# Performance work log

Hardware: AMD Instinct MI355X
Metric: run time of the kernel (lower is better)

Reference implementation:

```python
import jax, jax.numpy as jnp
import numpy as np

N_NODES = 100000
N_EDGES = 3200000
IN_CH = 128
HID = 32


def setup_inputs() -> dict:
    key = jax.random.key(0)
    ks = jax.random.split(key, 8)
    x = jax.random.normal(ks[0], (N_NODES, IN_CH), dtype=jnp.float32)
    edge_index = jax.random.randint(ks[1], (2, N_EDGES), 0, N_NODES, dtype=jnp.int64)
    # Glorot-ish scaled weights
    W1 = jax.random.normal(ks[2], (IN_CH, HID), dtype=jnp.float32) / np.sqrt(IN_CH)
    b1 = jnp.zeros((HID,), dtype=jnp.float32)
    W2 = jax.random.normal(ks[3], (HID, HID), dtype=jnp.float32) / np.sqrt(HID)
    b2 = jnp.zeros((HID,), dtype=jnp.float32)
    Wc = jax.random.normal(ks[4], (HID, 2), dtype=jnp.float32) / np.sqrt(HID)
    bc = jnp.zeros((2,), dtype=jnp.float32)
    return {"x": x, "edge_index": edge_index, "W1": W1, "b1": b1,
            "W2": W2, "b2": b2, "Wc": Wc, "bc": bc}


def _gcn_norm(edge_index, n_nodes):
    # PyG GCNConv default: add self-loops, symmetric normalization
    src, dst = edge_index[0], edge_index[1]
    loops = jnp.arange(n_nodes, dtype=src.dtype)
    src = jnp.concatenate([src, loops])
    dst = jnp.concatenate([dst, loops])
    deg = jax.ops.segment_sum(jnp.ones_like(dst, dtype=jnp.float32), dst,
                              num_segments=n_nodes)
    dis = jnp.where(deg > 0, jax.lax.rsqrt(deg), 0.0)  # deg^{-1/2}
    norm = dis[src] * dis[dst]                          # [E + N]
    return src, dst, norm


def _gcn_conv(x, W, b, src, dst, norm, n_nodes):
    h = x @ W                                   # [N, out] linear first (out <= in)
    msg = h[src] * norm[:, None]                # gather + scale  [E+N, out]
    out = jax.ops.segment_sum(msg, dst, num_segments=n_nodes)  # scatter-add
    return out + b


def reference(x, edge_index, W1, b1, W2, b2, Wc, bc):
    n = x.shape[0]
    src, dst, norm = _gcn_norm(edge_index, n)
    h = jax.nn.relu(_gcn_conv(x, W1, b1, src, dst, norm, n))
    h = jax.nn.relu(_gcn_conv(h, W2, b2, src, dst, norm, n))
    return h @ Wc + bc                          # [N, 2]
```

## Files before the change

kernel.cpp:

```cpp
#include <hip/hip_runtime.h>

#define NCH 32
#define INCH 128
#define SH 7
#define BNODES 128
#define CAP 4544
#define P1_CHUNK 8192
#define NBINS_PAD 1024
#define HCH 16

__device__ __forceinline__ unsigned int pack_bf16x2(float a, float b) {
  unsigned int ua = __float_as_uint(a);
  unsigned int ub = __float_as_uint(b);
  ua = (ua + 0x7FFFu + ((ua >> 16) & 1u)) >> 16;
  ub = (ub + 0x7FFFu + ((ub >> 16) & 1u)) & 0xFFFF0000u;
  return ub | ua;
}
__device__ __forceinline__ float lo_bf16(unsigned int u) { return __uint_as_float(u << 16); }
__device__ __forceinline__ float hi_bf16(unsigned int u) { return __uint_as_float(u & 0xFFFF0000u); }

__global__ void k_initcur(int* gcur, int nbk) {
  int i = blockIdx.x * blockDim.x + threadIdx.x;
  if (i < nbk) gcur[i] = i * CAP;
}

__global__ __launch_bounds__(256) void k_part(const int* __restrict__ ei, int* gcur,
                                              unsigned int* __restrict__ srcsb, int E) {
  __shared__ unsigned int sorted[P1_CHUNK];
  __shared__ int hist[NBINS_PAD];
  __shared__ int bbase[NBINS_PAD + 1];
  __shared__ int bfill[NBINS_PAD];
  __shared__ int wsums[4];
  const int tid = threadIdx.x;
  const int base = blockIdx.x * P1_CHUNK;
  const int cnt = min(P1_CHUNK, E - base);

  for (int i = tid; i < NBINS_PAD; i += 256) hist[i] = 0;
  __syncthreads();
  for (int i = tid; i < cnt; i += 256) {
    int d = ei[E + base + i];
    atomicAdd(&hist[d >> SH], 1);
  }
  __syncthreads();
  int c0 = hist[4 * tid], c1 = hist[4 * tid + 1], c2 = hist[4 * tid + 2], c3 = hist[4 * tid + 3];
  int s = c0 + c1 + c2 + c3;
  int lane = tid & 63, w = tid >> 6;
  int incl = s;
#pragma unroll
  for (int off = 1; off < 64; off <<= 1) {
    int t = __shfl_up(incl, off, 64);
    if (lane >= off) incl += t;
  }
  if (lane == 63) wsums[w] = incl;
  __syncthreads();
  int woff = 0;
  for (int i = 0; i < w; ++i) woff += wsums[i];
  int te = woff + incl - s;
  bbase[4 * tid] = te;                     bfill[4 * tid] = te;
  bbase[4 * tid + 1] = te + c0;            bfill[4 * tid + 1] = te + c0;
  bbase[4 * tid + 2] = te + c0 + c1;       bfill[4 * tid + 2] = te + c0 + c1;
  bbase[4 * tid + 3] = te + c0 + c1 + c2;  bfill[4 * tid + 3] = te + c0 + c1 + c2;
  if (tid == 255) bbase[NBINS_PAD] = te + s;
  __syncthreads();
  for (int i = tid; i < cnt; i += 256) {
    int d = ei[E + base + i];
    int srcv = ei[base + i];
    int b = d >> SH;
    int pos = atomicAdd(&bfill[b], 1);
    sorted[pos] = ((unsigned int)(d & (BNODES - 1)) << 17) | (unsigned int)srcv;
  }
  __syncthreads();
  for (int b = tid; b < NBINS_PAD; b += 256) {
    int c = bbase[b + 1] - bbase[b];
    hist[b] = (c > 0) ? atomicAdd(&gcur[b], c) : 0;
  }
  __syncthreads();
  for (int i = tid; i < cnt; i += 256) {
    int lo = 0, hi = NBINS_PAD - 1;
#pragma unroll
    for (int it = 0; it < 10; ++it) {
      int mid = (lo + hi + 1) >> 1;
      if (bbase[mid] <= i) lo = mid; else hi = mid - 1;
    }
    int gpos = hist[lo] + (i - bbase[lo]);
    if (gpos < (lo + 1) * CAP) srcsb[gpos] = sorted[i];
  }
}

__global__ __launch_bounds__(256) void k_bsort(const int* __restrict__ gcur,
                                               unsigned int* __restrict__ srcsb,
                                               int* __restrict__ rowbeg, int* __restrict__ rowend,
                                               float* __restrict__ dis, int N) {
  __shared__ unsigned int raw[CAP];
  __shared__ unsigned int sbuf[CAP];
  __shared__ int hist2[BNODES];
  __shared__ int sc[BNODES];
  __shared__ int fill2[BNODES];
  const int tid = threadIdx.x;
  const int bin = blockIdx.x;
  const int base = bin * CAP;
  int cnt = min(gcur[bin] - base, CAP);

  if (tid < BNODES) hist2[tid] = 0;
  for (int i = tid; i < cnt; i += 256) raw[i] = srcsb[base + i];
  __syncthreads();
  for (int i = tid; i < cnt; i += 256) atomicAdd(&hist2[raw[i] >> 17], 1);
  __syncthreads();
  int deg = (tid < BNODES) ? hist2[tid] : 0;
  if (tid < BNODES) sc[tid] = deg;
  __syncthreads();
  for (int off = 1; off < BNODES; off <<= 1) {
    int t = 0;
    if (tid < BNODES && tid >= off) t = sc[tid - off];
    __syncthreads();
    if (tid < BNODES) sc[tid] += t;
    __syncthreads();
  }
  int excl = 0;
  if (tid < BNODES) { excl = sc[tid] - deg; fill2[tid] = excl; }
  __syncthreads();
  for (int i = tid; i < cnt; i += 256) {
    unsigned int v = raw[i];
    int pos = atomicAdd(&fill2[v >> 17], 1);
    sbuf[pos] = v & 0x1FFFFu;
  }
  __syncthreads();
  for (int i = tid; i < cnt; i += 256) srcsb[base + i] = sbuf[i];
  if (tid < BNODES) {
    int n = bin * BNODES + tid;
    if (n < N) {
      rowbeg[n] = base + excl;
      rowend[n] = base + excl + deg;
      dis[n] = rsqrtf((float)(deg + 1));
    }
  }
}

__global__ __launch_bounds__(256) void k_gemm1(const float* __restrict__ x,
                                               const float* __restrict__ W1,
                                               const float* __restrict__ dis,
                                               unsigned int* __restrict__ hs, int N) {
  __shared__ float w[INCH * NCH];
  for (int i = threadIdx.x; i < INCH * NCH; i += blockDim.x) w[i] = W1[i];
  __syncthreads();
  int n = blockIdx.x * 16 + (threadIdx.x >> 4);
  int c2 = threadIdx.x & 15;
  if (n >= N) return;
  const float* xr = x + (size_t)n * INCH;
  float ax = 0.f, ay = 0.f;
#pragma unroll
  for (int k = 0; k < INCH; ++k) {
    float xv = xr[k];
    float2 ww = ((const float2*)(w + k * NCH))[c2];
    ax = fmaf(xv, ww.x, ax);
    ay = fmaf(xv, ww.y, ay);
  }
  float dn = dis[n];
  hs[(size_t)n * HCH + c2] = pack_bf16x2(ax * dn, ay * dn);
}

__global__ __launch_bounds__(256) void k_agg1g2(
    const int* __restrict__ rowbeg, const int* __restrict__ rowend,
    const unsigned int* __restrict__ srcs, const unsigned int* __restrict__ hs,
    const float* __restrict__ dis, const float* __restrict__ b1,
    const float* __restrict__ W2, unsigned int* __restrict__ hs2, int N) {
  __shared__ float w[NCH * NCH];
  for (int i = threadIdx.x; i < NCH * NCH; i += blockDim.x) w[i] = W2[i];
  __syncthreads();
  int n = blockIdx.x * 16 + (threadIdx.x >> 4);
  int c2 = threadIdx.x & 15;
  if (n >= N) return;
  int j = rowbeg[n], end = rowend[n];
  unsigned int su = hs[(size_t)n * HCH + c2];
  float ax = lo_bf16(su), ay = hi_bf16(su);
  for (; j + 8 <= end; j += 8) {
    unsigned int u0 = hs[(size_t)srcs[j] * HCH + c2];
    unsigned int u1 = hs[(size_t)srcs[j + 1] * HCH + c2];
    unsigned int u2 = hs[(size_t)srcs[j + 2] * HCH + c2];
    unsigned int u3 = hs[(size_t)srcs[j + 3] * HCH + c2];
    unsigned int u4 = hs[(size_t)srcs[j + 4] * HCH + c2];
    unsigned int u5 = hs[(size_t)srcs[j + 5] * HCH + c2];
    unsigned int u6 = hs[(size_t)srcs[j + 6] * HCH + c2];
    unsigned int u7 = hs[(size_t)srcs[j + 7] * HCH + c2];
    ax += ((lo_bf16(u0) + lo_bf16(u1)) + (lo_bf16(u2) + lo_bf16(u3))) +
          ((lo_bf16(u4) + lo_bf16(u5)) + (lo_bf16(u6) + lo_bf16(u7)));
    ay += ((hi_bf16(u0) + hi_bf16(u1)) + (hi_bf16(u2) + hi_bf16(u3))) +
          ((hi_bf16(u4) + hi_bf16(u5)) + (hi_bf16(u6) + hi_bf16(u7)));
  }
  for (; j < end; ++j) {
    unsigned int u = hs[(size_t)srcs[j] * HCH + c2];
    ax += lo_bf16(u);
    ay += hi_bf16(u);
  }
  float dn = dis[n];
  float v0 = fmaxf(fmaf(ax, dn, b1[2 * c2]), 0.f);
  float v1 = fmaxf(fmaf(ay, dn, b1[2 * c2 + 1]), 0.f);
  float o0 = 0.f, o1 = 0.f;
#pragma unroll
  for (int k2 = 0; k2 < 16; ++k2) {
    float a = __shfl(v0, k2, 16);
    float b = __shfl(v1, k2, 16);
    float2 wa = ((const float2*)(w + (2 * k2) * NCH))[c2];
    float2 wb = ((const float2*)(w + (2 * k2 + 1) * NCH))[c2];
    o0 = fmaf(a, wa.x, fmaf(b, wb.x, o0));
    o1 = fmaf(a, wa.y, fmaf(b, wb.y, o1));
  }
  hs2[(size_t)n * HCH + c2] = pack_bf16x2(o0 * dn, o1 * dn);
}

__global__ __launch_bounds__(256) void k_agg2h(
    const int* __restrict__ rowbeg, const int* __restrict__ rowend,
    const unsigned int* __restrict__ srcs, const unsigned int* __restrict__ hs2,
    const float* __restrict__ dis, const float* __restrict__ b2,
    const float* __restrict__ Wc, const float* __restrict__ bc,
    float* __restrict__ out, int N) {
  int n = blockIdx.x * 16 + (threadIdx.x >> 4);
  int c2 = threadIdx.x & 15;
  if (n >= N) return;
  int j = rowbeg[n], end = rowend[n];
  unsigned int su = hs2[(size_t)n * HCH + c2];
  float ax = lo_bf16(su), ay = hi_bf16(su);
  for (; j + 8 <= end; j += 8) {
    unsigned int u0 = hs2[(size_t)srcs[j] * HCH + c2];
    unsigned int u1 = hs2[(size_t)srcs[j + 1] * HCH + c2];
    unsigned int u2 = hs2[(size_t)srcs[j + 2] * HCH + c2];
    unsigned int u3 = hs2[(size_t)srcs[j + 3] * HCH + c2];
    unsigned int u4 = hs2[(size_t)srcs[j + 4] * HCH + c2];
    unsigned int u5 = hs2[(size_t)srcs[j + 5] * HCH + c2];
    unsigned int u6 = hs2[(size_t)srcs[j + 6] * HCH + c2];
    unsigned int u7 = hs2[(size_t)srcs[j + 7] * HCH + c2];
    ax += ((lo_bf16(u0) + lo_bf16(u1)) + (lo_bf16(u2) + lo_bf16(u3))) +
          ((lo_bf16(u4) + lo_bf16(u5)) + (lo_bf16(u6) + lo_bf16(u7)));
    ay += ((hi_bf16(u0) + hi_bf16(u1)) + (hi_bf16(u2) + hi_bf16(u3))) +
          ((hi_bf16(u4) + hi_bf16(u5)) + (hi_bf16(u6) + hi_bf16(u7)));
  }
  for (; j < end; ++j) {
    unsigned int u = hs2[(size_t)srcs[j] * HCH + c2];
    ax += lo_bf16(u);
    ay += hi_bf16(u);
  }
  float dn = dis[n];
  float v0 = fmaxf(fmaf(ax, dn, b2[2 * c2]), 0.f);
  float v1 = fmaxf(fmaf(ay, dn, b2[2 * c2 + 1]), 0.f);
  float s0 = v0 * Wc[(2 * c2) * 2 + 0] + v1 * Wc[(2 * c2 + 1) * 2 + 0];
  float s1 = v0 * Wc[(2 * c2) * 2 + 1] + v1 * Wc[(2 * c2 + 1) * 2 + 1];
#pragma unroll
  for (int off = 8; off > 0; off >>= 1) {
    s0 += __shfl_down(s0, off, 16);
    s1 += __shfl_down(s1, off, 16);
  }
  if (c2 == 0) {
    out[(size_t)n * 2 + 0] = s0 + bc[0];
    out[(size_t)n * 2 + 1] = s1 + bc[1];
  }
}

extern "C" void kernel_launch(void* const* d_in, const int* in_sizes, int n_in,
                              void* d_out, int out_size, void* d_ws, size_t ws_size,
                              hipStream_t stream) {
  const float* x  = (const float*)d_in[0];
  const int*   ei = (const int*)d_in[1];
  const float* W1 = (const float*)d_in[2];
  const float* b1 = (const float*)d_in[3];
  const float* W2 = (const float*)d_in[4];
  const float* b2 = (const float*)d_in[5];
  const float* Wc = (const float*)d_in[6];
  const float* bc = (const float*)d_in[7];
  float* out = (float*)d_out;

  const int N = in_sizes[0] / INCH;
  const int E = in_sizes[1] / 2;
  const int nbk = (N + BNODES - 1) / BNODES;

  float*        dis    = (float*)d_ws;
  int*          rowbeg = (int*)(dis + N);
  int*          rowend = rowbeg + N;
  int*          gcur   = rowend + N;
  unsigned int* srcsb  = (unsigned int*)(gcur + nbk);
  unsigned int* bufA   = srcsb + (size_t)nbk * CAP;
  unsigned int* bufB   = bufA + (size_t)N * HCH;

  const int bn = 256;
  const int gP1  = (E + P1_CHUNK - 1) / P1_CHUNK;
  const int gN16 = (N + 15) / 16;

  k_initcur<<<(nbk + bn - 1) / bn, bn, 0, stream>>>(gcur, nbk);
  k_part<<<gP1, bn, 0, stream>>>(ei, gcur, srcsb, E);
  k_bsort<<<nbk, bn, 0, stream>>>(gcur, srcsb, rowbeg, rowend, dis, N);

  k_gemm1<<<gN16, bn, 0, stream>>>(x, W1, dis, bufA, N);
  k_agg1g2<<<gN16, bn, 0, stream>>>(rowbeg, rowend, srcsb, bufA, dis, b1, W2, bufB, N);
  k_agg2h<<<gN16, bn, 0, stream>>>(rowbeg, rowend, srcsb, bufB, dis, b2, Wc, bc, out, N);
}
```

Measured before the change: 212.6 us.

## Split feature tables into channel halves to shrink gather working set

```diff
diff --git a/kernel.cpp b/kernel.cpp
--- a/kernel.cpp
+++ b/kernel.cpp
@@ -7,7 +7,7 @@
 #define CAP 4544
 #define P1_CHUNK 8192
 #define NBINS_PAD 1024
-#define HCH 16
+#define HB 8
 
 __device__ __forceinline__ unsigned int pack_bf16x2(float a, float b) {
   unsigned int ua = __float_as_uint(a);
@@ -139,7 +139,8 @@
 __global__ __launch_bounds__(256) void k_gemm1(const float* __restrict__ x,
                                                const float* __restrict__ W1,
                                                const float* __restrict__ dis,
-                                               unsigned int* __restrict__ hs, int N) {
+                                               unsigned int* __restrict__ hsA,
+                                               unsigned int* __restrict__ hsB, int N) {
   __shared__ float w[INCH * NCH];
   for (int i = threadIdx.x; i < INCH * NCH; i += blockDim.x) w[i] = W1[i];
   __syncthreads();
@@ -156,92 +157,85 @@
     ay = fmaf(xv, ww.y, ay);
   }
   float dn = dis[n];
-  hs[(size_t)n * HCH + c2] = pack_bf16x2(ax * dn, ay * dn);
-}
-
-__global__ __launch_bounds__(256) void k_agg1g2(
+  unsigned int p = pack_bf16x2(ax * dn, ay * dn);
+  if (c2 < 8) hsA[(size_t)n * HB + c2] = p;
+  else        hsB[(size_t)n * HB + (c2 - 8)] = p;
+}
+
+__global__ __launch_bounds__(256) void k_aggh(
     const int* __restrict__ rowbeg, const int* __restrict__ rowend,
-    const unsigned int* __restrict__ srcs, const unsigned int* __restrict__ hs,
-    const float* __restrict__ dis, const float* __restrict__ b1,
-    const float* __restrict__ W2, unsigned int* __restrict__ hs2, int N) {
-  __shared__ float w[NCH * NCH];
-  for (int i = threadIdx.x; i < NCH * NCH; i += blockDim.x) w[i] = W2[i];
-  __syncthreads();
-  int n = blockIdx.x * 16 + (threadIdx.x >> 4);
-  int c2 = threadIdx.x & 15;
+    const unsigned int* __restrict__ srcs, const unsigned int* __restrict__ tbl,
+    float2* __restrict__ acc, int N) {
+  int n = blockIdx.x * 32 + (threadIdx.x >> 3);
+  int c = threadIdx.x & 7;
   if (n >= N) return;
   int j = rowbeg[n], end = rowend[n];
-  unsigned int su = hs[(size_t)n * HCH + c2];
+  unsigned int su = tbl[(size_t)n * HB + c];
   float ax = lo_bf16(su), ay = hi_bf16(su);
   for (; j + 8 <= end; j += 8) {
-    unsigned int u0 = hs[(size_t)srcs[j] * HCH + c2];
-    unsigned int u1 = hs[(size_t)srcs[j + 1] * HCH + c2];
-    unsigned int u2 = hs[(size_t)srcs[j + 2] * HCH + c2];
-    unsigned int u3 = hs[(size_t)srcs[j + 3] * HCH + c2];
-    unsigned int u4 = hs[(size_t)srcs[j + 4] * HCH + c2];
-    unsigned int u5 = hs[(size_t)srcs[j + 5] * HCH + c2];
-    unsigned int u6 = hs[(size_t)srcs[j + 6] * HCH + c2];
-    unsigned int u7 = hs[(size_t)srcs[j + 7] * HCH + c2];
+    unsigned int u0 = tbl[(size_t)srcs[j] * HB + c];
+    unsigned int u1 = tbl[(size_t)srcs[j + 1] * HB + c];
+    unsigned int u2 = tbl[(size_t)srcs[j + 2] * HB + c];
+    unsigned int u3 = tbl[(size_t)srcs[j + 3] * HB + c];
+    unsigned int u4 = tbl[(size_t)srcs[j + 4] * HB + c];
+    unsigned int u5 = tbl[(size_t)srcs[j + 5] * HB + c];
+    unsigned int u6 = tbl[(size_t)srcs[j + 6] * HB + c];
+    unsigned int u7 = tbl[(size_t)srcs[j + 7] * HB + c];
     ax += ((lo_bf16(u0) + lo_bf16(u1)) + (lo_bf16(u2) + lo_bf16(u3))) +
           ((lo_bf16(u4) + lo_bf16(u5)) + (lo_bf16(u6) + lo_bf16(u7)));
     ay += ((hi_bf16(u0) + hi_bf16(u1)) + (hi_bf16(u2) + hi_bf16(u3))) +
           ((hi_bf16(u4) + hi_bf16(u5)) + (hi_bf16(u6) + hi_bf16(u7)));
   }
   for (; j < end; ++j) {
-    unsigned int u = hs[(size_t)srcs[j] * HCH + c2];
+    unsigned int u = tbl[(size_t)srcs[j] * HB + c];
     ax += lo_bf16(u);
     ay += hi_bf16(u);
   }
+  acc[(size_t)n * HB + c] = make_float2(ax, ay);
+}
+
+__global__ __launch_bounds__(256) void k_mlp2(
+    const float2* __restrict__ accA, const float2* __restrict__ accB,
+    const float* __restrict__ dis, const float* __restrict__ b1,
+    const float* __restrict__ W2, unsigned int* __restrict__ hs2A,
+    unsigned int* __restrict__ hs2B, int N) {
+  __shared__ float w[NCH * NCH];
+  for (int i = threadIdx.x; i < NCH * NCH; i += blockDim.x) w[i] = W2[i];
+  __syncthreads();
+  int n = blockIdx.x * 16 + (threadIdx.x >> 4);
+  int c2 = threadIdx.x & 15;
+  if (n >= N) return;
+  float2 a = (c2 < 8) ? accA[(size_t)n * HB + c2] : accB[(size_t)n * HB + (c2 - 8)];
   float dn = dis[n];
-  float v0 = fmaxf(fmaf(ax, dn, b1[2 * c2]), 0.f);
-  float v1 = fmaxf(fmaf(ay, dn, b1[2 * c2 + 1]), 0.f);
+  float v0 = fmaxf(fmaf(a.x, dn, b1[2 * c2]), 0.f);
+  float v1 = fmaxf(fmaf(a.y, dn, b1[2 * c2 + 1]), 0.f);
   float o0 = 0.f, o1 = 0.f;
 #pragma unroll
   for (int k2 = 0; k2 < 16; ++k2) {
-    float a = __shfl(v0, k2, 16);
-    float b = __shfl(v1, k2, 16);
+    float va = __shfl(v0, k2, 16);
+    float vb = __shfl(v1, k2, 16);
     float2 wa = ((const float2*)(w + (2 * k2) * NCH))[c2];
     float2 wb = ((const float2*)(w + (2 * k2 + 1) * NCH))[c2];
-    o0 = fmaf(a, wa.x, fmaf(b, wb.x, o0));
-    o1 = fmaf(a, wa.y, fmaf(b, wb.y, o1));
-  }
-  hs2[(size_t)n * HCH + c2] = pack_bf16x2(o0 * dn, o1 * dn);
-}
-
-__global__ __launch_bounds__(256) void k_agg2h(
-    const int* __restrict__ rowbeg, const int* __restrict__ rowend,
-    const unsigned int* __restrict__ srcs, const unsigned int* __restrict__ hs2,
+    o0 = fmaf(va, wa.x, fmaf(vb, wb.x, o0));
+    o1 = fmaf(va, wa.y, fmaf(vb, wb.y, o1));
+  }
+  unsigned int p = pack_bf16x2(o0 * dn, o1 * dn);
+  if (c2 < 8) hs2A[(size_t)n * HB + c2] = p;
+  else        hs2B[(size_t)n * HB + (c2 - 8)] = p;
+}
+
+__global__ __launch_bounds__(256) void k_head(
+    const float2* __restrict__ accA, const float2* __restrict__ accB,
     const float* __restrict__ dis, const float* __restrict__ b2,
     const float* __restrict__ Wc, const float* __restrict__ bc,
     float* __restrict__ out, int N) {
   int n = blockIdx.x * 16 + (threadIdx.x >> 4);
   int c2 = threadIdx.x & 15;
   if (n >= N) return;
-  int j = rowbeg[n], end = rowend[n];
-  unsigned int su = hs2[(size_t)n * HCH + c2];
-  float ax = lo_bf16(su), ay = hi_bf16(su);
-  for (; j + 8 <= end; j += 8) {
-    unsigned int u0 = hs2[(size_t)srcs[j] * HCH + c2];
-    unsigned int u1 = hs2[(size_t)srcs[j + 1] * HCH + c2];
-    unsigned int u2 = hs2[(size_t)srcs[j + 2] * HCH + c2];
-    unsigned int u3 = hs2[(size_t)srcs[j + 3] * HCH + c2];
-    unsigned int u4 = hs2[(size_t)srcs[j + 4] * HCH + c2];
-    unsigned int u5 = hs2[(size_t)srcs[j + 5] * HCH + c2];
-    unsigned int u6 = hs2[(size_t)srcs[j + 6] * HCH + c2];
-    unsigned int u7 = hs2[(size_t)srcs[j + 7] * HCH + c2];
-    ax += ((lo_bf16(u0) + lo_bf16(u1)) + (lo_bf16(u2) + lo_bf16(u3))) +
-          ((lo_bf16(u4) + lo_bf16(u5)) + (lo_bf16(u6) + lo_bf16(u7)));
-    ay += ((hi_bf16(u0) + hi_bf16(u1)) + (hi_bf16(u2) + hi_bf16(u3))) +
-          ((hi_bf16(u4) + hi_bf16(u5)) + (hi_bf16(u6) + hi_bf16(u7)));
-  }
-  for (; j < end; ++j) {
-    unsigned int u = hs2[(size_t)srcs[j] * HCH + c2];
-    ax += lo_bf16(u);
-    ay += hi_bf16(u);
-  }
+  float2 a = (c2 < 8) ? accA[(size_t)n * HB + c2] : accB[(size_t)n * HB + (c2 - 8)];
   float dn = dis[n];
-  float v0 = fmaxf(fmaf(ax, dn, b2[2 * c2]), 0.f);
-  float v1 = fmaxf(fmaf(ay, dn, b2[2 * c2 + 1]), 0.f);
+  float v0 = fmaxf(fmaf(a.x, dn, b2[2 * c2]), 0.f);
+  float v1 = fmaxf(fmaf(a.y, dn, b2[2 * c2 + 1]), 0.f);
   float s0 = v0 * Wc[(2 * c2) * 2 + 0] + v1 * Wc[(2 * c2 + 1) * 2 + 0];
   float s1 = v0 * Wc[(2 * c2) * 2 + 1] + v1 * Wc[(2 * c2 + 1) * 2 + 1];
 #pragma unroll
@@ -276,19 +270,29 @@
   int*          rowbeg = (int*)(dis + N);
   int*          rowend = rowbeg + N;
   int*          gcur   = rowend + N;
-  unsigned int* srcsb  = (unsigned int*)(gcur + nbk);
-  unsigned int* bufA   = srcsb + (size_t)nbk * CAP;
-  unsigned int* bufB   = bufA + (size_t)N * HCH;
+  unsigned int* srcsb  = (unsigned int*)(gcur + nbk + 2);
+  unsigned int* hsA    = srcsb + (size_t)nbk * CAP;
+  unsigned int* hsB    = hsA + (size_t)N * HB;
+  float2*       accA   = (float2*)(hsB + (size_t)N * HB);
+  float2*       accB   = accA + (size_t)N * HB;
+  unsigned int* hs2A   = (unsigned int*)(accB + (size_t)N * HB);
+  unsigned int* hs2B   = hs2A + (size_t)N * HB;
 
   const int bn = 256;
   const int gP1  = (E + P1_CHUNK - 1) / P1_CHUNK;
   const int gN16 = (N + 15) / 16;
+  const int gN32 = (N + 31) / 32;
 
   k_initcur<<<(nbk + bn - 1) / bn, bn, 0, stream>>>(gcur, nbk);
   k_part<<<gP1, bn, 0, stream>>>(ei, gcur, srcsb, E);
   k_bsort<<<nbk, bn, 0, stream>>>(gcur, srcsb, rowbeg, rowend, dis, N);
 
-  k_gemm1<<<gN16, bn, 0, stream>>>(x, W1, dis, bufA, N);
-  k_agg1g2<<<gN16, bn, 0, stream>>>(rowbeg, rowend, srcsb, bufA, dis, b1, W2, bufB, N);
-  k_agg2h<<<gN16, bn, 0, stream>>>(rowbeg, rowend, srcsb, bufB, dis, b2, Wc, bc, out, N);
-}
+  k_gemm1<<<gN16, bn, 0, stream>>>(x, W1, dis, hsA, hsB, N);
+  k_aggh<<<gN32, bn, 0, stream>>>(rowbeg, rowend, srcsb, hsA, accA, N);
+  k_aggh<<<gN32, bn, 0, stream>>>(rowbeg, rowend, srcsb, hsB, accB, N);
+  k_mlp2<<<gN16, bn, 0, stream>>>(accA, accB, dis, b1, W2, hs2A, hs2B, N);
+
+  k_aggh<<<gN32, bn, 0, stream>>>(rowbeg, rowend, srcsb, hs2A, accA, N);
+  k_aggh<<<gN32, bn, 0, stream>>>(rowbeg, rowend, srcsb, hs2B, accB, N);
+  k_head<<<gN16, bn, 0, stream>>>(accA, accB, dis, b2, Wc, bc, out, N);
+}
```

After: 230.5 us. 8.4% more time.
